# Kernel optimization log

Hardware: AMD Instinct MI355X
Metric: run time of the kernel (lower is better)

## Reference

```python
import jax, jax.numpy as jnp
import numpy as np

N_NODES = 50000
N_EDGES = 800000
IN_CH = 128
HEADS = 4
OUT_CH = 4
N_GRAPHS = 64
NEG_SLOPE = 0.2  # GATv2Conv default leaky_relu slope
EPS = 1e-5       # GraphNorm eps


def _seg_sum(x, seg, n):
    return jax.ops.segment_sum(x, seg, num_segments=n)


def _seg_mean(x, seg, n):
    s = _seg_sum(x, seg, n)
    cnt = _seg_sum(jnp.ones((seg.shape[0],), x.dtype), seg, n)
    return s / jnp.maximum(cnt, 1.0)[:, None]


def gatv2_conv(x, src, dst, n, w_l, w_r, att, bias, heads, out_ch, concat):
    # x: [N, F_in]; src/dst: [E_tot] (self-loops already appended)
    x_l = (x @ w_l).reshape(n, heads, out_ch)
    x_r = (x @ w_r).reshape(n, heads, out_ch)
    m = jax.nn.leaky_relu(x_l[src] + x_r[dst], NEG_SLOPE)   # [E, H, C]
    e = jnp.einsum('ehc,hc->eh', m, att)                    # [E, H]
    # softmax over incoming edges of each destination node
    e_max = jax.ops.segment_max(e, dst, num_segments=n)     # [N, H]
    w = jnp.exp(e - e_max[dst])
    denom = _seg_sum(w, dst, n)                             # [N, H]
    alpha = w / denom[dst]
    out = _seg_sum(alpha[:, :, None] * x_l[src], dst, n)    # [N, H, C]
    out = out.reshape(n, heads * out_ch) if concat else out.mean(axis=1)
    return out + bias


def graph_norm(x, batch, weight, bias, mean_scale, n_graphs):
    mu = _seg_mean(x, batch, n_graphs)                      # [G, C]
    out = x - mu[batch] * mean_scale
    var = _seg_mean(out * out, batch, n_graphs)
    return out / jnp.sqrt(var[batch] + EPS) * weight + bias


def setup_inputs() -> dict:
    key = jax.random.key(0)
    ks = jax.random.split(key, 20)
    H = HEADS
    d = {}
    d['x'] = jax.random.normal(ks[0], (N_NODES, IN_CH), dtype=jnp.float32)
    d['edge_index'] = jax.random.randint(ks[1], (2, N_EDGES), 0, N_NODES, dtype=jnp.int32)
    d['batch'] = jnp.sort(jax.random.randint(ks[2], (N_NODES,), 0, N_GRAPHS, dtype=jnp.int32))
    def glorot(k, shape):
        fan = shape[0] + shape[-1]
        return jax.random.normal(k, shape, dtype=jnp.float32) * np.sqrt(2.0 / fan).astype(np.float32)
    # layer 1: in 128 -> 32 per head, concat -> 128
    d['w_l1'] = glorot(ks[3], (IN_CH, H * 32)); d['w_r1'] = glorot(ks[4], (IN_CH, H * 32))
    d['att1'] = glorot(ks[5], (H, 32)); d['b1'] = jnp.zeros((H * 32,), jnp.float32)
    d['gn1_w'] = jnp.ones((H * 32,), jnp.float32); d['gn1_b'] = jnp.zeros((H * 32,), jnp.float32); d['gn1_s'] = jnp.ones((H * 32,), jnp.float32)
    # layer 2: 128 -> 16 per head, concat -> 64
    d['w_l2'] = glorot(ks[6], (H * 32, H * 16)); d['w_r2'] = glorot(ks[7], (H * 32, H * 16))
    d['att2'] = glorot(ks[8], (H, 16)); d['b2'] = jnp.zeros((H * 16,), jnp.float32)
    d['gn2_w'] = jnp.ones((H * 16,), jnp.float32); d['gn2_b'] = jnp.zeros((H * 16,), jnp.float32); d['gn2_s'] = jnp.ones((H * 16,), jnp.float32)
    # layer 3: 64 -> 8 per head, mean over heads -> 8
    d['w_l3'] = glorot(ks[9], (H * 16, H * 8)); d['w_r3'] = glorot(ks[10], (H * 16, H * 8))
    d['att3'] = glorot(ks[11], (H, 8)); d['b3'] = jnp.zeros((8,), jnp.float32)
    d['gn3_w'] = jnp.ones((8,), jnp.float32); d['gn3_b'] = jnp.zeros((8,), jnp.float32); d['gn3_s'] = jnp.ones((8,), jnp.float32)
    d['lin_w'] = glorot(ks[12], (8, OUT_CH)); d['lin_b'] = jnp.zeros((OUT_CH,), jnp.float32)
    return d


def reference(x, edge_index, batch,
              w_l1, w_r1, att1, b1, gn1_w, gn1_b, gn1_s,
              w_l2, w_r2, att2, b2, gn2_w, gn2_b, gn2_s,
              w_l3, w_r3, att3, b3, gn3_w, gn3_b, gn3_s,
              lin_w, lin_b):
    n = x.shape[0]
    loop = jnp.arange(n, dtype=edge_index.dtype)
    src = jnp.concatenate([edge_index[0], loop])  # add_self_loops=True (PyG default)
    dst = jnp.concatenate([edge_index[1], loop])
    h = gatv2_conv(x, src, dst, n, w_l1, w_r1, att1, b1, HEADS, 32, True)
    h = jax.nn.relu(graph_norm(h, batch, gn1_w, gn1_b, gn1_s, N_GRAPHS))
    h = gatv2_conv(h, src, dst, n, w_l2, w_r2, att2, b2, HEADS, 16, True)
    h = jax.nn.relu(graph_norm(h, batch, gn2_w, gn2_b, gn2_s, N_GRAPHS))
    h = gatv2_conv(h, src, dst, n, w_l3, w_r3, att3, b3, HEADS, 8, False)
    h = jax.nn.relu(graph_norm(h, batch, gn3_w, gn3_b, gn3_s, N_GRAPHS))
    features = _seg_mean(h, batch, N_GRAPHS)  # global_mean_pool -> [G, 8]
    logits = features @ lin_w + lin_b         # [G, OUT_CH]
    return (logits, features)
```

## Files before the change

### kernel.cpp

```cpp
#include <hip/hip_runtime.h>
#include <hip/hip_fp16.h>
#include <math.h>

#define NN 50000
#define NE 800000
#define ET (NE + NN)
#define NG 64
#define H 4
#define NBK 196
#define CH 4096
#define SB ((ET + CH - 1) / CH)

typedef _Float16 half8 __attribute__((ext_vector_type(8)));
typedef _Float16 hv2 __attribute__((ext_vector_type(2)));
typedef float floatx4 __attribute__((ext_vector_type(4)));


__device__ __forceinline__ void edge_sd(int e, const int* __restrict__ ei, int& s, int& d) {
    if (e < NE) { s = ei[e]; d = ei[NE + e]; } else { s = e - NE; d = s; }
}

__global__ __launch_bounds__(256) void k_bhist(const int* __restrict__ ei, int* __restrict__ bcnt) {
    __shared__ int hist[NBK];
    int b0 = blockIdx.x, tid = threadIdx.x;
    for (int i = tid; i < NBK; i += 256) hist[i] = 0;
    __syncthreads();
#pragma unroll
    for (int pass = 0; pass < CH / 256; ++pass) {
        int e = b0 * CH + pass * 256 + tid;
        if (e < ET) {
            int d = (e < NE) ? ei[NE + e] : (e - NE);
            atomicAdd(&hist[d >> 8], 1);
        }
    }
    __syncthreads();
    if (tid < NBK) bcnt[tid * SB + b0] = hist[tid];
}

__global__ __launch_bounds__(256) void k_bscanA(const int* __restrict__ bcnt, int* __restrict__ boff,
                                                int* __restrict__ tot) {
    __shared__ int lds[256];
    int b = blockIdx.x, t = threadIdx.x;
    int v = (t < SB) ? bcnt[b * SB + t] : 0;
    lds[t] = v;
    __syncthreads();
    for (int off = 1; off < 256; off <<= 1) {
        int y = (t >= off) ? lds[t - off] : 0;
        __syncthreads();
        lds[t] += y;
        __syncthreads();
    }
    if (t < SB) boff[b * SB + t] = lds[t] - v;
    if (t == 255) tot[b] = lds[255];
}

__global__ __launch_bounds__(256) void k_bscanB(const int* __restrict__ tot, int* __restrict__ ebase,
                                                const int* __restrict__ bpos, int* __restrict__ cnt) {
    __shared__ int lds[256];
    int t = threadIdx.x;
    int v = (t < NBK) ? tot[t] : 0;
    lds[t] = v;
    __syncthreads();
    for (int off = 1; off < 256; off <<= 1) {
        int y = (t >= off) ? lds[t - off] : 0;
        __syncthreads();
        lds[t] += y;
        __syncthreads();
    }
    if (t < NBK) ebase[t] = lds[t] - v;
    if (t == 0) ebase[NBK] = ET;
    if (t < NG) cnt[t] = bpos[t + 1] - bpos[t];
}

__global__ __launch_bounds__(256) void k_bounds(const int* __restrict__ batch, int* __restrict__ bpos) {
    int i = blockIdx.x * 256 + threadIdx.x;
    if (i >= NN) return;
    int cur = batch[i];
    int prev = (i == 0) ? -1 : batch[i - 1];
    for (int g = prev + 1; g <= cur; ++g) bpos[g] = i;
    if (i == NN - 1)
        for (int g = cur + 1; g <= NG; ++g) bpos[g] = NN;
}

__global__ __launch_bounds__(256) void k_bscatter(const int* __restrict__ ei, const int* __restrict__ ebase,
                                                  const int* __restrict__ boff, unsigned int* __restrict__ ebuf) {
    __shared__ int cur[NBK];
    int b0 = blockIdx.x, tid = threadIdx.x;
    for (int i = tid; i < NBK; i += 256) cur[i] = ebase[i] + boff[i * SB + b0];
    __syncthreads();
#pragma unroll
    for (int pass = 0; pass < CH / 256; ++pass) {
        int e = b0 * CH + pass * 256 + tid;
        if (e < ET) {
            int s, d;
            edge_sd(e, ei, s, d);
            int pos = atomicAdd(&cur[d >> 8], 1);
            ebuf[pos] = ((unsigned)s << 16) | (unsigned)(d & 255);
        }
    }
}

__global__ __launch_bounds__(256) void k_bsort(const unsigned int* __restrict__ ebuf,
                                               const int* __restrict__ ebase,
                                               int* __restrict__ rowptr, unsigned short* __restrict__ colsrc) {
    __shared__ int cnt2[256];
    __shared__ int sc[256];
    __shared__ int cur2[256];
    int b = blockIdx.x, t = threadIdx.x;
    int base = ebase[b], n = ebase[b + 1] - base;
    cnt2[t] = 0;
    __syncthreads();
    for (int i = t; i < n; i += 256) atomicAdd(&cnt2[ebuf[base + i] & 255], 1);
    __syncthreads();
    int v = cnt2[t];
    sc[t] = v;
    __syncthreads();
    for (int off = 1; off < 256; off <<= 1) {
        int y = (t >= off) ? sc[t - off] : 0;
        __syncthreads();
        sc[t] += y;
        __syncthreads();
    }
    int excl = sc[t] - v;
    int d = b * 256 + t;
    if (d < NN) rowptr[d] = base + excl;
    if (b == 0 && t == 0) rowptr[NN] = ET;
    cur2[t] = excl;
    __syncthreads();
    for (int i = t; i < n; i += 256) {
        unsigned u = ebuf[base + i];
        int pos = atomicAdd(&cur2[u & 255], 1);
        colsrc[base + pos] = (unsigned short)(u >> 16);
    }
}


template <int K, int M2>
__device__ __forceinline__ void wprep_fn(int chunk, const float* __restrict__ Wl, const float* __restrict__ Wr,
                                         _Float16* __restrict__ Wfrag) {
    constexpr int MTOT = 2 * M2, NT = MTOT / 16;
    if (chunk >= MTOT * K / 8) return;
    int lane = chunk & 63, tt = chunk >> 6;
    int t = tt % NT, kt = tt / NT;
    int n = t * 16 + (lane & 15);
    int kb = kt * 32 + (lane >> 4) * 8;
    const float* src = (n < M2) ? (Wl + n) : (Wr + (n - M2));
    half8 h;
#pragma unroll
    for (int j = 0; j < 8; ++j) h[j] = (_Float16)src[(size_t)(kb + j) * M2];
    *(half8*)(Wfrag + (size_t)chunk * 8) = h;
}

__global__ __launch_bounds__(256) void k_wprep_all(const float* __restrict__ Wl1, const float* __restrict__ Wr1,
                                                   const float* __restrict__ Wl2, const float* __restrict__ Wr2,
                                                   const float* __restrict__ Wl3, const float* __restrict__ Wr3,
                                                   _Float16* __restrict__ Wf1, _Float16* __restrict__ Wf2,
                                                   _Float16* __restrict__ Wf3) {
    int b = blockIdx.x, t = threadIdx.x;
    if (b < 16)      wprep_fn<128, 128>(b * 256 + t, Wl1, Wr1, Wf1);
    else if (b < 24) wprep_fn<128, 64>((b - 16) * 256 + t, Wl2, Wr2, Wf2);
    else             wprep_fn<64, 32>((b - 24) * 256 + t, Wl3, Wr3, Wf3);
}


template <typename AT>
__device__ __forceinline__ half8 load_a8(const AT* __restrict__ ap) {
    if constexpr (__is_same(AT, _Float16)) {
        return *(const half8*)ap;
    } else {
        const float4* p = (const float4*)ap;
        float4 a = p[0], b = p[1];
        half8 h;
        h[0] = (_Float16)a.x; h[1] = (_Float16)a.y; h[2] = (_Float16)a.z; h[3] = (_Float16)a.w;
        h[4] = (_Float16)b.x; h[5] = (_Float16)b.y; h[6] = (_Float16)b.z; h[7] = (_Float16)b.w;
        return h;
    }
}

template <int K, int M2, typename AT>
__global__ __launch_bounds__(256) void k_dualgemm(const AT* __restrict__ Ain,
                                                  const _Float16* __restrict__ Wfrag,
                                                  __half* __restrict__ Ol, float* __restrict__ Or) {
    constexpr int MTOT = 2 * M2;
    constexpr int NT = MTOT / 16;
    constexpr int KT = K / 32;
    int tid = threadIdx.x;
    int wid = tid >> 6, lane = tid & 63;
    int q = lane >> 4, l15 = lane & 15;
    int r0 = blockIdx.x * 64 + wid * 16;
    int arow = min(r0 + l15, NN - 1);
    const AT* ap = Ain + (size_t)arow * K + q * 8;

    floatx4 acc[NT];
#pragma unroll
    for (int t = 0; t < NT; ++t) acc[t] = (floatx4){0.f, 0.f, 0.f, 0.f};

#pragma unroll
    for (int kt = 0; kt < KT; ++kt) {
        half8 a8 = load_a8<AT>(ap + kt * 32);
        const _Float16* wp = Wfrag + ((size_t)(kt * NT) * 64 + lane) * 8;
#pragma unroll
        for (int t = 0; t < NT; ++t) {
            half8 b8 = *(const half8*)(wp + (size_t)t * 64 * 8);
            acc[t] = __builtin_amdgcn_mfma_f32_16x16x32_f16(a8, b8, acc[t], 0, 0, 0);
        }
    }

#pragma unroll
    for (int t = 0; t < NT; ++t) {
        int cn = t * 16 + l15;
#pragma unroll
        for (int reg = 0; reg < 4; ++reg) {
            int r = r0 + q * 4 + reg;
            if (r < NN) {
                if (cn < M2) Ol[(size_t)r * M2 + cn] = __float2half(acc[t][reg]);
                else         Or[(size_t)r * M2 + (cn - M2)] = acc[t][reg];
            }
        }
    }
}


template <int CP> struct HVec { hv2 h2[CP / 2]; };

template <int CP>
__device__ __forceinline__ HVec<CP> load_hv(const __half* __restrict__ p) {
    HVec<CP> r;
    if constexpr (CP == 8) { float4 t = *(const float4*)p; r = *(HVec<CP>*)&t; }
    else if constexpr (CP == 4) { float2 t = *(const float2*)p; r = *(HVec<CP>*)&t; }
    else { r.h2[0] = *(const hv2*)p; }
    return r;
}

template <int C, int EP, bool CONCAT>
__global__ __launch_bounds__(256, 8) void k_attn(const __half* __restrict__ xl, const float* __restrict__ xr,
                                                 const int* __restrict__ rowptr,
                                                 const unsigned short* __restrict__ colsrc,
                                                 const float* __restrict__ att, const float* __restrict__ bias,
                                                 float* __restrict__ out) {
    constexpr int CP = C / EP;
    int t = blockIdx.x * 256 + threadIdx.x;
    int part = t & (EP - 1);
    int nh = t >> 2;
    if (nh >= NN * H) return;
    int node = nh >> 2, h = nh & 3;
    int cbase = h * C + part * CP;
    hv2 xrr2[CP / 2], attv2[CP / 2];
    float acc[CP];
    {
        const float* p = xr + (size_t)node * (H * C) + cbase;
        const float* q = att + cbase;
#pragma unroll
        for (int j = 0; j < CP / 2; ++j) {
            xrr2[j] = (hv2){(_Float16)p[2 * j], (_Float16)p[2 * j + 1]};
            attv2[j] = (hv2){(_Float16)q[2 * j], (_Float16)q[2 * j + 1]};
        }
#pragma unroll
        for (int c = 0; c < CP; ++c) acc[c] = 0.f;
    }
    float denom = 0.f;
    int beg = rowptr[node], end = rowptr[node + 1];

    auto process = [&](const HVec<CP>& xv) {
        float part_s = 0.f;
#pragma unroll
        for (int j = 0; j < CP / 2; ++j) {
            hv2 z = xv.h2[j] + xrr2[j];
            hv2 l = __builtin_elementwise_max(z, z * (_Float16)0.2f);
            part_s = __builtin_amdgcn_fdot2(l, attv2[j], part_s, false);
        }
        float score = part_s;
#pragma unroll
        for (int mask = 1; mask < EP; mask <<= 1) score += __shfl_xor(score, mask, 64);
        float w = __expf(score);
        denom += w;
        const _Float16* xh = (const _Float16*)&xv;
#pragma unroll
        for (int c = 0; c < CP; ++c) acc[c] = fmaf(w, (float)xh[c], acc[c]);
    };

    int idx = beg;
    for (; idx + 4 <= end; idx += 4) {
        int s0 = colsrc[idx], s1 = colsrc[idx + 1], s2 = colsrc[idx + 2], s3 = colsrc[idx + 3];
        HVec<CP> xv0 = load_hv<CP>(xl + (size_t)s0 * (H * C) + cbase);
        HVec<CP> xv1 = load_hv<CP>(xl + (size_t)s1 * (H * C) + cbase);
        HVec<CP> xv2 = load_hv<CP>(xl + (size_t)s2 * (H * C) + cbase);
        HVec<CP> xv3 = load_hv<CP>(xl + (size_t)s3 * (H * C) + cbase);
        process(xv0);
        process(xv1);
        process(xv2);
        process(xv3);
    }
    for (; idx < end; ++idx) {
        int s = colsrc[idx];
        HVec<CP> xv = load_hv<CP>(xl + (size_t)s * (H * C) + cbase);
        process(xv);
    }

    float inv = 1.f / denom;
    float* op = out + (size_t)node * (H * C) + cbase;
    float v[CP];
#pragma unroll
    for (int c = 0; c < CP; ++c) {
        v[c] = acc[c] * inv;
        if (CONCAT) v[c] += bias[cbase + c];
    }
    if constexpr (CP == 8) {
        *(float4*)(op) = make_float4(v[0], v[1], v[2], v[3]);
        *(float4*)(op + 4) = make_float4(v[4], v[5], v[6], v[7]);
    } else if constexpr (CP == 4) {
        *(float4*)(op) = make_float4(v[0], v[1], v[2], v[3]);
    } else {
        *(float2*)(op) = make_float2(v[0], v[1]);
    }
}


template <int LOGC, int SPLIT>
__global__ __launch_bounds__(256) void k_gnred2(const float* __restrict__ h, const int* __restrict__ bpos,
                                                float* __restrict__ sum, float* __restrict__ sumsq) {
    constexpr int C = 1 << LOGC;
    constexpr int RG = 256 >> LOGC;
    int g = blockIdx.x / SPLIT, s = blockIdx.x % SPLIT;
    int c = threadIdx.x & (C - 1);
    int rg = threadIdx.x >> LOGC;
    int b0 = bpos[g], b1 = bpos[g + 1];
    int n = b1 - b0;
    int seg = (n + SPLIT - 1) / SPLIT;
    int r0 = b0 + s * seg;
    int r1 = min(r0 + seg, b1);
    float sv = 0.f, ssv = 0.f;
    for (int r = r0 + rg; r < r1; r += RG) {
        float x = h[(size_t)r * C + c];
        sv += x; ssv += x * x;
    }
    __shared__ float ls[256], lss[256];
    ls[threadIdx.x] = sv; lss[threadIdx.x] = ssv;
    __syncthreads();
    for (int off = 128; off >= C; off >>= 1) {
        if (threadIdx.x < off) {
            ls[threadIdx.x] += ls[threadIdx.x + off];
            lss[threadIdx.x] += lss[threadIdx.x + off];
        }
        __syncthreads();
    }
    if (threadIdx.x < C) {
        atomicAdd(&sum[g * C + threadIdx.x], ls[threadIdx.x]);
        atomicAdd(&sumsq[g * C + threadIdx.x], lss[threadIdx.x]);
    }
}

__global__ __launch_bounds__(256) void k_gnnorm(float* __restrict__ h, const int* __restrict__ batch,
                                                const float* __restrict__ sum, const float* __restrict__ sumsq,
                                                const int* __restrict__ cnt, const float* __restrict__ w,
                                                const float* __restrict__ b, const float* __restrict__ ms,
                                                int logC, __half* __restrict__ h16) {
    int C = 1 << logC;
    int i = blockIdx.x * 256 + threadIdx.x;
    if (i >= NN * C) return;
    int nd = i >> logC, c = i & (C - 1);
    int g = batch[nd];
    float cg = fmaxf((float)cnt[g], 1.f);
    float mu = sum[g * C + c] / cg;
    float ex2 = sumsq[g * C + c] / cg;
    float s_ = ms[c];
    float var = ex2 - (2.f * s_ - s_ * s_) * mu * mu;
    float y = (h[i] - mu * s_) * rsqrtf(var + 1e-5f) * w[c] + b[c];
    y = fmaxf(y, 0.f);
    if (h16) h16[i] = __float2half(y);
    else     h[i] = y;
}


template <int SPLIT>
__global__ __launch_bounds__(256) void k_headgn(const float* __restrict__ tmp, const float* __restrict__ b3,
                                                const int* __restrict__ bpos, float* __restrict__ Af,
                                                float* __restrict__ sum, float* __restrict__ sumsq) {
    constexpr int C = 8, RG = 32;
    int g = blockIdx.x / SPLIT, s = blockIdx.x % SPLIT;
    int c = threadIdx.x & 7;
    int rg = threadIdx.x >> 3;
    int b0 = bpos[g], b1 = bpos[g + 1];
    int n = b1 - b0;
    int seg = (n + SPLIT - 1) / SPLIT;
    int r0 = b0 + s * seg;
    int r1 = min(r0 + seg, b1);
    float bias = b3[c];
    float sv = 0.f, ssv = 0.f;
    for (int r = r0 + rg; r < r1; r += RG) {
        const float* p = tmp + (size_t)r * 32 + c;
        float v = 0.25f * (p[0] + p[8] + p[16] + p[24]) + bias;
        Af[(size_t)r * C + c] = v;
        sv += v; ssv += v * v;
    }
    __shared__ float ls[256], lss[256];
    ls[threadIdx.x] = sv; lss[threadIdx.x] = ssv;
    __syncthreads();
    for (int off = 128; off >= C; off >>= 1) {
        if (threadIdx.x < off) {
            ls[threadIdx.x] += ls[threadIdx.x + off];
            lss[threadIdx.x] += lss[threadIdx.x + off];
        }
        __syncthreads();
    }
    if (threadIdx.x < C) {
        atomicAdd(&sum[g * C + threadIdx.x], ls[threadIdx.x]);
        atomicAdd(&sumsq[g * C + threadIdx.x], lss[threadIdx.x]);
    }
}


template <int SPLIT>
__global__ __launch_bounds__(256) void k_gnpool(const float* __restrict__ Af, const int* __restrict__ bpos,
                                                const float* __restrict__ sum, const float* __restrict__ sumsq,
                                                const int* __restrict__ cnt, const float* __restrict__ w,
                                                const float* __restrict__ b, const float* __restrict__ ms,
                                                float* __restrict__ pool) {
    constexpr int C = 8, RG = 32;
    int g = blockIdx.x / SPLIT, s = blockIdx.x % SPLIT;
    int c = threadIdx.x & 7;
    int rg = threadIdx.x >> 3;
    int b0 = bpos[g], b1 = bpos[g + 1];
    int n = b1 - b0;
    int seg = (n + SPLIT - 1) / SPLIT;
    int r0 = b0 + s * seg;
    int r1 = min(r0 + seg, b1);
    float cg = fmaxf((float)cnt[g], 1.f);
    float mu = sum[g * C + c] / cg;
    float ex2 = sumsq[g * C + c] / cg;
    float s_ = ms[c];
    float var = ex2 - (2.f * s_ - s_ * s_) * mu * mu;
    float rs = rsqrtf(var + 1e-5f) * w[c];
    float bb = b[c], mus = mu * s_;
    float pv = 0.f;
    for (int r = r0 + rg; r < r1; r += RG) {
        float y = fmaxf((Af[(size_t)r * C + c] - mus) * rs + bb, 0.f);
        pv += y;
    }
    __shared__ float ls[256];
    ls[threadIdx.x] = pv;
    __syncthreads();
    for (int off = 128; off >= C; off >>= 1) {
        if (threadIdx.x < off) ls[threadIdx.x] += ls[threadIdx.x + off];
        __syncthreads();
    }
    if (threadIdx.x < C) atomicAdd(&pool[g * C + threadIdx.x], ls[threadIdx.x]);
}


__global__ __launch_bounds__(512) void k_final(const float* __restrict__ pool, const int* __restrict__ cnt,
                                               const float* __restrict__ lw, const float* __restrict__ lb,
                                               float* __restrict__ outp) {
    __shared__ float feat[512];
    int t = threadIdx.x;
    int g = t >> 3;
    float f = pool[t] / fmaxf((float)cnt[g], 1.f);
    feat[t] = f;
    outp[256 + t] = f;
    __syncthreads();
    if (t < 256) {
        int g2 = t >> 2, o = t & 3;
        float a = lb[o];
#pragma unroll
        for (int cc = 0; cc < 8; ++cc) a += feat[g2 * 8 + cc] * lw[cc * 4 + o];
        outp[t] = a;
    }
}


extern "C" void kernel_launch(void* const* d_in, const int* in_sizes, int n_in,
                              void* d_out, int out_size, void* d_ws, size_t ws_size,
                              hipStream_t stream) {
    const float* x    = (const float*)d_in[0];
    const int*   ei   = (const int*)d_in[1];
    const int*   batch= (const int*)d_in[2];
    const float *w_l1 = (const float*)d_in[3],  *w_r1 = (const float*)d_in[4];
    const float *att1 = (const float*)d_in[5],  *b1   = (const float*)d_in[6];
    const float *gn1w = (const float*)d_in[7],  *gn1b = (const float*)d_in[8],  *gn1s = (const float*)d_in[9];
    const float *w_l2 = (const float*)d_in[10], *w_r2 = (const float*)d_in[11];
    const float *att2 = (const float*)d_in[12], *b2   = (const float*)d_in[13];
    const float *gn2w = (const float*)d_in[14], *gn2b = (const float*)d_in[15], *gn2s = (const float*)d_in[16];
    const float *w_l3 = (const float*)d_in[17], *w_r3 = (const float*)d_in[18];
    const float *att3 = (const float*)d_in[19], *b3   = (const float*)d_in[20];
    const float *gn3w = (const float*)d_in[21], *gn3b = (const float*)d_in[22], *gn3s = (const float*)d_in[23];
    const float *lw   = (const float*)d_in[24], *lb   = (const float*)d_in[25];

    char* ws = (char*)d_ws;
    size_t off = 0;
    auto alloc = [&](size_t bytes) -> void* {
        void* p = ws + off;
        off += (bytes + 255) & ~(size_t)255;
        return p;
    };
    __half* Ah  = (__half*)alloc((size_t)NN * 128 * 2);
    __half* Xh  = (__half*)alloc((size_t)NN * 128 * 2);
    float*  B   = (float*)alloc((size_t)NN * 128 * 4);
    float*  Cb  = (float*)alloc((size_t)NN * 64 * 4);
    float*  Af  = (float*)alloc((size_t)NN * 8 * 4);
    _Float16* Wf1 = (_Float16*)alloc((size_t)256 * 128 * 2);
    _Float16* Wf2 = (_Float16*)alloc((size_t)128 * 128 * 2);
    _Float16* Wf3 = (_Float16*)alloc((size_t)64 * 64 * 2);
    int* rowptr = (int*)alloc((size_t)(NN + 1) * 4);
    unsigned short* colsrc = (unsigned short*)alloc((size_t)ET * 2);
    unsigned int* ebuf = (unsigned int*)alloc((size_t)ET * 4);
    int* bcnt   = (int*)alloc((size_t)NBK * SB * 4);
    int* boff   = (int*)alloc((size_t)NBK * SB * 4);
    int* tot    = (int*)alloc((size_t)NBK * 4);
    int* ebase  = (int*)alloc((size_t)(NBK + 1) * 4);
    int* bpos   = (int*)alloc((size_t)(NG + 1) * 4);
    int* cnt    = (int*)alloc((size_t)NG * 4);
    char* zbase = ws + off;
    float* sum1 = (float*)alloc((size_t)NG * 128 * 4);
    float* sq1  = (float*)alloc((size_t)NG * 128 * 4);
    float* sum2 = (float*)alloc((size_t)NG * 64 * 4);
    float* sq2  = (float*)alloc((size_t)NG * 64 * 4);
    float* sum3 = (float*)alloc((size_t)NG * 8 * 4);
    float* sq3  = (float*)alloc((size_t)NG * 8 * 4);
    float* pool = (float*)alloc((size_t)NG * 8 * 4);
    size_t zbytes = (size_t)((ws + off) - zbase);
    (void)hipMemsetAsync(zbase, 0, zbytes, stream);

    k_wprep_all<<<26, 256, 0, stream>>>(w_l1, w_r1, w_l2, w_r2, w_l3, w_r3, Wf1, Wf2, Wf3);
    k_bounds<<<(NN + 255) / 256, 256, 0, stream>>>(batch, bpos);
    k_bhist<<<SB, 256, 0, stream>>>(ei, bcnt);
    k_bscanA<<<NBK, 256, 0, stream>>>(bcnt, boff, tot);
    k_bscanB<<<1, 256, 0, stream>>>(tot, ebase, bpos, cnt);
    k_bscatter<<<SB, 256, 0, stream>>>(ei, ebase, boff, ebuf);
    k_bsort<<<NBK, 256, 0, stream>>>(ebuf, ebase, rowptr, colsrc);

    int gA4 = (NN * H * 4) / 256;
    int gD  = (NN + 63) / 64;

    k_dualgemm<128, 128, float><<<gD, 256, 0, stream>>>(x, Wf1, Ah, B);
    k_attn<32, 4, true><<<gA4, 256, 0, stream>>>(Ah, B, rowptr, colsrc, att1, b1, B);
    k_gnred2<7, 8><<<NG * 8, 256, 0, stream>>>(B, bpos, sum1, sq1);
    k_gnnorm<<<(NN * 128 + 255) / 256, 256, 0, stream>>>(B, batch, sum1, sq1, cnt, gn1w, gn1b, gn1s, 7, Xh);

    k_dualgemm<128, 64, _Float16><<<gD, 256, 0, stream>>>((const _Float16*)Xh, Wf2, Ah, Cb);
    k_attn<16, 4, true><<<gA4, 256, 0, stream>>>(Ah, Cb, rowptr, colsrc, att2, b2, Cb);
    k_gnred2<6, 8><<<NG * 8, 256, 0, stream>>>(Cb, bpos, sum2, sq2);
    k_gnnorm<<<(NN * 64 + 255) / 256, 256, 0, stream>>>(Cb, batch, sum2, sq2, cnt, gn2w, gn2b, gn2s, 6, Xh);

    k_dualgemm<64, 32, _Float16><<<gD, 256, 0, stream>>>((const _Float16*)Xh, Wf3, Ah, B);
    k_attn<8, 4, false><<<gA4, 256, 0, stream>>>(Ah, B, rowptr, colsrc, att3, nullptr, B);
    k_headgn<8><<<NG * 8, 256, 0, stream>>>(B, b3, bpos, Af, sum3, sq3);
    k_gnpool<8><<<NG * 8, 256, 0, stream>>>(Af, bpos, sum3, sq3, cnt, gn3w, gn3b, gn3s, pool);
    k_final<<<1, 512, 0, stream>>>(pool, cnt, lw, lb, (float*)d_out);
}
```

Measured before the change: 336.3 us.

## Fuse prep kernels, fold bucket scan into scatter/sort, tune attention edge-parallel split

Merges weight prep, graph-boundary computation and the edge bucket histogram into a single launch. It also removes the single-block scan kernel by recomputing the bucket prefix sum redundantly inside the scatter and sort blocks, and derives graph counts directly from bpos. Layers 2 and 3 now use fewer threads per node-head in the attention kernel (EP 2 and 1), which gives each thread more channels and fewer shuffle reductions. The trade-off is redundant scans in every block and lower thread-level parallelism in the later attention layers.

```diff
diff --git a/kernel.cpp b/kernel.cpp
--- a/kernel.cpp
+++ b/kernel.cpp
@@ -14,125 +14,6 @@
 typedef _Float16 half8 __attribute__((ext_vector_type(8)));
 typedef _Float16 hv2 __attribute__((ext_vector_type(2)));
 typedef float floatx4 __attribute__((ext_vector_type(4)));
-
-
-__device__ __forceinline__ void edge_sd(int e, const int* __restrict__ ei, int& s, int& d) {
-    if (e < NE) { s = ei[e]; d = ei[NE + e]; } else { s = e - NE; d = s; }
-}
-
-__global__ __launch_bounds__(256) void k_bhist(const int* __restrict__ ei, int* __restrict__ bcnt) {
-    __shared__ int hist[NBK];
-    int b0 = blockIdx.x, tid = threadIdx.x;
-    for (int i = tid; i < NBK; i += 256) hist[i] = 0;
-    __syncthreads();
-#pragma unroll
-    for (int pass = 0; pass < CH / 256; ++pass) {
-        int e = b0 * CH + pass * 256 + tid;
-        if (e < ET) {
-            int d = (e < NE) ? ei[NE + e] : (e - NE);
-            atomicAdd(&hist[d >> 8], 1);
-        }
-    }
-    __syncthreads();
-    if (tid < NBK) bcnt[tid * SB + b0] = hist[tid];
-}
-
-__global__ __launch_bounds__(256) void k_bscanA(const int* __restrict__ bcnt, int* __restrict__ boff,
-                                                int* __restrict__ tot) {
-    __shared__ int lds[256];
-    int b = blockIdx.x, t = threadIdx.x;
-    int v = (t < SB) ? bcnt[b * SB + t] : 0;
-    lds[t] = v;
-    __syncthreads();
-    for (int off = 1; off < 256; off <<= 1) {
-        int y = (t >= off) ? lds[t - off] : 0;
-        __syncthreads();
-        lds[t] += y;
-        __syncthreads();
-    }
-    if (t < SB) boff[b * SB + t] = lds[t] - v;
-    if (t == 255) tot[b] = lds[255];
-}
-
-__global__ __launch_bounds__(256) void k_bscanB(const int* __restrict__ tot, int* __restrict__ ebase,
-                                                const int* __restrict__ bpos, int* __restrict__ cnt) {
-    __shared__ int lds[256];
-    int t = threadIdx.x;
-    int v = (t < NBK) ? tot[t] : 0;
-    lds[t] = v;
-    __syncthreads();
-    for (int off = 1; off < 256; off <<= 1) {
-        int y = (t >= off) ? lds[t - off] : 0;
-        __syncthreads();
-        lds[t] += y;
-        __syncthreads();
-    }
-    if (t < NBK) ebase[t] = lds[t] - v;
-    if (t == 0) ebase[NBK] = ET;
-    if (t < NG) cnt[t] = bpos[t + 1] - bpos[t];
-}
-
-__global__ __launch_bounds__(256) void k_bounds(const int* __restrict__ batch, int* __restrict__ bpos) {
-    int i = blockIdx.x * 256 + threadIdx.x;
-    if (i >= NN) return;
-    int cur = batch[i];
-    int prev = (i == 0) ? -1 : batch[i - 1];
-    for (int g = prev + 1; g <= cur; ++g) bpos[g] = i;
-    if (i == NN - 1)
-        for (int g = cur + 1; g <= NG; ++g) bpos[g] = NN;
-}
-
-__global__ __launch_bounds__(256) void k_bscatter(const int* __restrict__ ei, const int* __restrict__ ebase,
-                                                  const int* __restrict__ boff, unsigned int* __restrict__ ebuf) {
-    __shared__ int cur[NBK];
-    int b0 = blockIdx.x, tid = threadIdx.x;
-    for (int i = tid; i < NBK; i += 256) cur[i] = ebase[i] + boff[i * SB + b0];
-    __syncthreads();
-#pragma unroll
-    for (int pass = 0; pass < CH / 256; ++pass) {
-        int e = b0 * CH + pass * 256 + tid;
-        if (e < ET) {
-            int s, d;
-            edge_sd(e, ei, s, d);
-            int pos = atomicAdd(&cur[d >> 8], 1);
-            ebuf[pos] = ((unsigned)s << 16) | (unsigned)(d & 255);
-        }
-    }
-}
-
-__global__ __launch_bounds__(256) void k_bsort(const unsigned int* __restrict__ ebuf,
-                                               const int* __restrict__ ebase,
-                                               int* __restrict__ rowptr, unsigned short* __restrict__ colsrc) {
-    __shared__ int cnt2[256];
-    __shared__ int sc[256];
-    __shared__ int cur2[256];
-    int b = blockIdx.x, t = threadIdx.x;
-    int base = ebase[b], n = ebase[b + 1] - base;
-    cnt2[t] = 0;
-    __syncthreads();
-    for (int i = t; i < n; i += 256) atomicAdd(&cnt2[ebuf[base + i] & 255], 1);
-    __syncthreads();
-    int v = cnt2[t];
-    sc[t] = v;
-    __syncthreads();
-    for (int off = 1; off < 256; off <<= 1) {
-        int y = (t >= off) ? sc[t - off] : 0;
-        __syncthreads();
-        sc[t] += y;
-        __syncthreads();
-    }
-    int excl = sc[t] - v;
-    int d = b * 256 + t;
-    if (d < NN) rowptr[d] = base + excl;
-    if (b == 0 && t == 0) rowptr[NN] = ET;
-    cur2[t] = excl;
-    __syncthreads();
-    for (int i = t; i < n; i += 256) {
-        unsigned u = ebuf[base + i];
-        int pos = atomicAdd(&cur2[u & 255], 1);
-        colsrc[base + pos] = (unsigned short)(u >> 16);
-    }
-}
 
 
 template <int K, int M2>
@@ -151,15 +32,141 @@
     *(half8*)(Wfrag + (size_t)chunk * 8) = h;
 }
 
-__global__ __launch_bounds__(256) void k_wprep_all(const float* __restrict__ Wl1, const float* __restrict__ Wr1,
-                                                   const float* __restrict__ Wl2, const float* __restrict__ Wr2,
-                                                   const float* __restrict__ Wl3, const float* __restrict__ Wr3,
-                                                   _Float16* __restrict__ Wf1, _Float16* __restrict__ Wf2,
-                                                   _Float16* __restrict__ Wf3) {
+
+__global__ __launch_bounds__(256) void k_prep(const float* __restrict__ Wl1, const float* __restrict__ Wr1,
+                                              const float* __restrict__ Wl2, const float* __restrict__ Wr2,
+                                              const float* __restrict__ Wl3, const float* __restrict__ Wr3,
+                                              _Float16* __restrict__ Wf1, _Float16* __restrict__ Wf2,
+                                              _Float16* __restrict__ Wf3,
+                                              const int* __restrict__ batch, int* __restrict__ bpos,
+                                              const int* __restrict__ ei, int* __restrict__ bcnt) {
     int b = blockIdx.x, t = threadIdx.x;
-    if (b < 16)      wprep_fn<128, 128>(b * 256 + t, Wl1, Wr1, Wf1);
-    else if (b < 24) wprep_fn<128, 64>((b - 16) * 256 + t, Wl2, Wr2, Wf2);
-    else             wprep_fn<64, 32>((b - 24) * 256 + t, Wl3, Wr3, Wf3);
+    if (b < 16) { wprep_fn<128, 128>(b * 256 + t, Wl1, Wr1, Wf1); return; }
+    if (b < 24) { wprep_fn<128, 64>((b - 16) * 256 + t, Wl2, Wr2, Wf2); return; }
+    if (b < 26) { wprep_fn<64, 32>((b - 24) * 256 + t, Wl3, Wr3, Wf3); return; }
+    if (b < 26 + NBK) {
+        int i = (b - 26) * 256 + t;
+        if (i >= NN) return;
+        int cur = batch[i];
+        int prev = (i == 0) ? -1 : batch[i - 1];
+        for (int g = prev + 1; g <= cur; ++g) bpos[g] = i;
+        if (i == NN - 1)
+            for (int g = cur + 1; g <= NG; ++g) bpos[g] = NN;
+        return;
+    }
+    __shared__ int hist[NBK];
+    int b0 = b - 26 - NBK;
+    for (int i = t; i < NBK; i += 256) hist[i] = 0;
+    __syncthreads();
+#pragma unroll
+    for (int pass = 0; pass < CH / 256; ++pass) {
+        int e = b0 * CH + pass * 256 + t;
+        if (e < ET) {
+            int d = (e < NE) ? ei[NE + e] : (e - NE);
+            atomicAdd(&hist[d >> 8], 1);
+        }
+    }
+    __syncthreads();
+    if (t < NBK) bcnt[t * SB + b0] = hist[t];
+}
+
+
+__global__ __launch_bounds__(256) void k_bscanA(const int* __restrict__ bcnt, int* __restrict__ boff,
+                                                int* __restrict__ tot) {
+    __shared__ int lds[256];
+    int b = blockIdx.x, t = threadIdx.x;
+    int v = (t < SB) ? bcnt[b * SB + t] : 0;
+    lds[t] = v;
+    __syncthreads();
+    for (int off = 1; off < 256; off <<= 1) {
+        int y = (t >= off) ? lds[t - off] : 0;
+        __syncthreads();
+        lds[t] += y;
+        __syncthreads();
+    }
+    if (t < SB) boff[b * SB + t] = lds[t] - v;
+    if (t == 255) tot[b] = lds[255];
+}
+
+
+__device__ __forceinline__ void edge_sd(int e, const int* __restrict__ ei, int& s, int& d) {
+    if (e < NE) { s = ei[e]; d = ei[NE + e]; } else { s = e - NE; d = s; }
+}
+
+__global__ __launch_bounds__(256) void k_bscatter(const int* __restrict__ ei, const int* __restrict__ tot,
+                                                  const int* __restrict__ boff, unsigned int* __restrict__ ebuf) {
+    __shared__ int eb[256];
+    __shared__ int cur[NBK];
+    int b0 = blockIdx.x, t = threadIdx.x;
+    int v = (t < NBK) ? tot[t] : 0;
+    eb[t] = v;
+    __syncthreads();
+    for (int off = 1; off < 256; off <<= 1) {
+        int y = (t >= off) ? eb[t - off] : 0;
+        __syncthreads();
+        eb[t] += y;
+        __syncthreads();
+    }
+    if (t < NBK) cur[t] = (eb[t] - v) + boff[t * SB + b0];
+    __syncthreads();
+#pragma unroll
+    for (int pass = 0; pass < CH / 256; ++pass) {
+        int e = b0 * CH + pass * 256 + t;
+        if (e < ET) {
+            int s, d;
+            edge_sd(e, ei, s, d);
+            int pos = atomicAdd(&cur[d >> 8], 1);
+            ebuf[pos] = ((unsigned)s << 16) | (unsigned)(d & 255);
+        }
+    }
+}
+
+
+__global__ __launch_bounds__(256) void k_bsort(const unsigned int* __restrict__ ebuf,
+                                               const int* __restrict__ tot,
+                                               int* __restrict__ rowptr, unsigned short* __restrict__ colsrc) {
+    __shared__ int eb[256];
+    __shared__ int sbase;
+    __shared__ int cnt2[256];
+    __shared__ int sc[256];
+    __shared__ int cur2[256];
+    int b = blockIdx.x, t = threadIdx.x;
+    int v = (t < NBK) ? tot[t] : 0;
+    eb[t] = v;
+    __syncthreads();
+    for (int off = 1; off < 256; off <<= 1) {
+        int y = (t >= off) ? eb[t - off] : 0;
+        __syncthreads();
+        eb[t] += y;
+        __syncthreads();
+    }
+    if (t == b) sbase = eb[t] - v;
+    __syncthreads();
+    int base = sbase, n = tot[b];
+    cnt2[t] = 0;
+    __syncthreads();
+    for (int i = t; i < n; i += 256) atomicAdd(&cnt2[ebuf[base + i] & 255], 1);
+    __syncthreads();
+    int cv = cnt2[t];
+    sc[t] = cv;
+    __syncthreads();
+    for (int off = 1; off < 256; off <<= 1) {
+        int y = (t >= off) ? sc[t - off] : 0;
+        __syncthreads();
+        sc[t] += y;
+        __syncthreads();
+    }
+    int excl = sc[t] - cv;
+    int d = b * 256 + t;
+    if (d < NN) rowptr[d] = base + excl;
+    if (b == 0 && t == 0) rowptr[NN] = ET;
+    cur2[t] = excl;
+    __syncthreads();
+    for (int i = t; i < n; i += 256) {
+        unsigned u = ebuf[base + i];
+        int pos = atomicAdd(&cur2[u & 255], 1);
+        colsrc[base + pos] = (unsigned short)(u >> 16);
+    }
 }
 
 
@@ -239,9 +246,10 @@
                                                  const float* __restrict__ att, const float* __restrict__ bias,
                                                  float* __restrict__ out) {
     constexpr int CP = C / EP;
+    constexpr int LEP = (EP == 4) ? 2 : ((EP == 2) ? 1 : 0);
     int t = blockIdx.x * 256 + threadIdx.x;
     int part = t & (EP - 1);
-    int nh = t >> 2;
+    int nh = t >> LEP;
     if (nh >= NN * H) return;
     int node = nh >> 2, h = nh & 3;
     int cbase = h * C + part * CP;
@@ -352,7 +360,7 @@
 
 __global__ __launch_bounds__(256) void k_gnnorm(float* __restrict__ h, const int* __restrict__ batch,
                                                 const float* __restrict__ sum, const float* __restrict__ sumsq,
-                                                const int* __restrict__ cnt, const float* __restrict__ w,
+                                                const int* __restrict__ bpos, const float* __restrict__ w,
                                                 const float* __restrict__ b, const float* __restrict__ ms,
                                                 int logC, __half* __restrict__ h16) {
     int C = 1 << logC;
@@ -360,7 +368,7 @@
     if (i >= NN * C) return;
     int nd = i >> logC, c = i & (C - 1);
     int g = batch[nd];
-    float cg = fmaxf((float)cnt[g], 1.f);
+    float cg = fmaxf((float)(bpos[g + 1] - bpos[g]), 1.f);
     float mu = sum[g * C + c] / cg;
     float ex2 = sumsq[g * C + c] / cg;
     float s_ = ms[c];
@@ -413,7 +421,7 @@
 template <int SPLIT>
 __global__ __launch_bounds__(256) void k_gnpool(const float* __restrict__ Af, const int* __restrict__ bpos,
                                                 const float* __restrict__ sum, const float* __restrict__ sumsq,
-                                                const int* __restrict__ cnt, const float* __restrict__ w,
+                                                const float* __restrict__ w,
                                                 const float* __restrict__ b, const float* __restrict__ ms,
                                                 float* __restrict__ pool) {
     constexpr int C = 8, RG = 32;
@@ -425,7 +433,7 @@
     int seg = (n + SPLIT - 1) / SPLIT;
     int r0 = b0 + s * seg;
     int r1 = min(r0 + seg, b1);
-    float cg = fmaxf((float)cnt[g], 1.f);
+    float cg = fmaxf((float)n, 1.f);
     float mu = sum[g * C + c] / cg;
     float ex2 = sumsq[g * C + c] / cg;
     float s_ = ms[c];
@@ -448,13 +456,13 @@
 }
 
 
-__global__ __launch_bounds__(512) void k_final(const float* __restrict__ pool, const int* __restrict__ cnt,
+__global__ __launch_bounds__(512) void k_final(const float* __restrict__ pool, const int* __restrict__ bpos,
                                                const float* __restrict__ lw, const float* __restrict__ lb,
                                                float* __restrict__ outp) {
     __shared__ float feat[512];
     int t = threadIdx.x;
     int g = t >> 3;
-    float f = pool[t] / fmaxf((float)cnt[g], 1.f);
+    float f = pool[t] / fmaxf((float)(bpos[g + 1] - bpos[g]), 1.f);
     feat[t] = f;
     outp[256 + t] = f;
     __syncthreads();
@@ -506,9 +514,7 @@
     int* bcnt   = (int*)alloc((size_t)NBK * SB * 4);
     int* boff   = (int*)alloc((size_t)NBK * SB * 4);
     int* tot    = (int*)alloc((size_t)NBK * 4);
-    int* ebase  = (int*)alloc((size_t)(NBK + 1) * 4);
     int* bpos   = (int*)alloc((size_t)(NG + 1) * 4);
-    int* cnt    = (int*)alloc((size_t)NG * 4);
     char* zbase = ws + off;
     float* sum1 = (float*)alloc((size_t)NG * 128 * 4);
     float* sq1  = (float*)alloc((size_t)NG * 128 * 4);
@@ -520,30 +526,30 @@
     size_t zbytes = (size_t)((ws + off) - zbase);
     (void)hipMemsetAsync(zbase, 0, zbytes, stream);
 
-    k_wprep_all<<<26, 256, 0, stream>>>(w_l1, w_r1, w_l2, w_r2, w_l3, w_r3, Wf1, Wf2, Wf3);
-    k_bounds<<<(NN + 255) / 256, 256, 0, stream>>>(batch, bpos);
-    k_bhist<<<SB, 256, 0, stream>>>(ei, bcnt);
+    k_prep<<<26 + NBK + SB, 256, 0, stream>>>(w_l1, w_r1, w_l2, w_r2, w_l3, w_r3, Wf1, Wf2, Wf3,
+                                              batch, bpos, ei, bcnt);
     k_bscanA<<<NBK, 256, 0, stream>>>(bcnt, boff, tot);
-    k_bscanB<<<1, 256, 0, stream>>>(tot, ebase, bpos, cnt);
-    k_bscatter<<<SB, 256, 0, stream>>>(ei, ebase, boff, ebuf);
-    k_bsort<<<NBK, 256, 0, stream>>>(ebuf, ebase, rowptr, colsrc);
-
-    int gA4 = (NN * H * 4) / 256;
+    k_bscatter<<<SB, 256, 0, stream>>>(ei, tot, boff, ebuf);
+    k_bsort<<<NBK, 256, 0, stream>>>(ebuf, tot, rowptr, colsrc);
+
+    int gA1 = (NN * H * 4) / 256;
+    int gA2 = (NN * H * 2 + 255) / 256;
+    int gA3 = (NN * H + 255) / 256;
     int gD  = (NN + 63) / 64;
 
     k_dualgemm<128, 128, float><<<gD, 256, 0, stream>>>(x, Wf1, Ah, B);
-    k_attn<32, 4, true><<<gA4, 256, 0, stream>>>(Ah, B, rowptr, colsrc, att1, b1, B);
+    k_attn<32, 4, true><<<gA1, 256, 0, stream>>>(Ah, B, rowptr, colsrc, att1, b1, B);
     k_gnred2<7, 8><<<NG * 8, 256, 0, stream>>>(B, bpos, sum1, sq1);
-    k_gnnorm<<<(NN * 128 + 255) / 256, 256, 0, stream>>>(B, batch, sum1, sq1, cnt, gn1w, gn1b, gn1s, 7, Xh);
+    k_gnnorm<<<(NN * 128 + 255) / 256, 256, 0, stream>>>(B, batch, sum1, sq1, bpos, gn1w, gn1b, gn1s, 7, Xh);
 
     k_dualgemm<128, 64, _Float16><<<gD, 256, 0, stream>>>((const _Float16*)Xh, Wf2, Ah, Cb);
-    k_attn<16, 4, true><<<gA4, 256, 0, stream>>>(Ah, Cb, rowptr, colsrc, att2, b2, Cb);
+    k_attn<16, 2, true><<<gA2, 256, 0, stream>>>(Ah, Cb, rowptr, colsrc, att2, b2, Cb);
     k_gnred2<6, 8><<<NG * 8, 256, 0, stream>>>(Cb, bpos, sum2, sq2);
-    k_gnnorm<<<(NN * 64 + 255) / 256, 256, 0, stream>>>(Cb, batch, sum2, sq2, cnt, gn2w, gn2b, gn2s, 6, Xh);
+    k_gnnorm<<<(NN * 64 + 255) / 256, 256, 0, stream>>>(Cb, batch, sum2, sq2, bpos, gn2w, gn2b, gn2s, 6, Xh);
 
     k_dualgemm<64, 32, _Float16><<<gD, 256, 0, stream>>>((const _Float16*)Xh, Wf3, Ah, B);
-    k_attn<8, 4, false><<<gA4, 256, 0, stream>>>(Ah, B, rowptr, colsrc, att3, nullptr, B);
+    k_attn<8, 1, false><<<gA3, 256, 0, stream>>>(Ah, B, rowptr, colsrc, att3, nullptr, B);
     k_headgn<8><<<NG * 8, 256, 0, stream>>>(B, b3, bpos, Af, sum3, sq3);
-    k_gnpool<8><<<NG * 8, 256, 0, stream>>>(Af, bpos, sum3, sq3, cnt, gn3w, gn3b, gn3s, pool);
-    k_final<<<1, 512, 0, stream>>>(pool, cnt, lw, lb, (float*)d_out);
-}
+    k_gnpool<8><<<NG * 8, 256, 0, stream>>>(Af, bpos, sum3, sq3, gn3w, gn3b, gn3s, pool);
+    k_final<<<1, 512, 0, stream>>>(pool, bpos, lw, lb, (float*)d_out);
+}
```

New measurement: 324.6 us. 3.5% less time.
